# Optimization experiments

Hardware: AMD Instinct MI355X
Metric: run time of the kernel (lower is better)

Reference implementation:

```python
import jax, jax.numpy as jnp
import numpy as np

EMBED = 1024
HEADS = 16
HEAD_DIM = EMBED // HEADS
N, L = 2, 2048


def setup_inputs() -> dict:
    key = jax.random.key(0)
    ks = jax.random.split(key, 9)
    s = 0.02
    return {
        "values": jax.random.normal(ks[0], (N, L, EMBED), jnp.float32),
        "key": jax.random.normal(ks[1], (N, L, EMBED), jnp.float32),
        "query": jax.random.normal(ks[2], (N, L, EMBED), jnp.float32),
        "mask": jnp.ones((N, 1, 1, L), jnp.int32),
        "Wv": jax.random.normal(ks[3], (HEAD_DIM, HEAD_DIM), jnp.float32) * s,
        "Wk": jax.random.normal(ks[4], (HEAD_DIM, HEAD_DIM), jnp.float32) * s,
        "Wq": jax.random.normal(ks[5], (HEAD_DIM, HEAD_DIM), jnp.float32) * s,
        "bq": jax.random.normal(ks[6], (HEAD_DIM,), jnp.float32) * s,
        "Wo": jax.random.normal(ks[7], (EMBED, EMBED), jnp.float32) * s,
        "bo": jax.random.normal(ks[8], (EMBED,), jnp.float32) * s,
    }


def reference(values, key, query, mask, Wv, Wk, Wq, bq, Wo, bo):
    n, q_len, E = query.shape
    D = Wv.shape[0]
    H = E // D
    # split heads: (N, len, H, D)
    v = values.reshape(n, -1, H, D)
    k = key.reshape(n, -1, H, D)
    q = query.reshape(n, q_len, H, D)
    # per-head linear projections (torch Linear: x @ W.T [+ b])
    v = jnp.einsum("nlhd,ed->nlhe", v, Wv)
    k = jnp.einsum("nlhd,ed->nlhe", k, Wk)
    q = jnp.einsum("nlhd,ed->nlhe", q, Wq) + bq
    # scores: (N, H, q_len, k_len)
    energy = jnp.einsum("nqhd,nkhd->nhqk", q, k)
    energy = jnp.where(mask == 0, jnp.float32(-1e20), energy)
    # NOTE: original scales by sqrt(embed_size), not sqrt(head_dim)
    attn = jax.nn.softmax(energy / jnp.sqrt(jnp.float32(E)), axis=-1)
    out = jnp.einsum("nhqk,nkhd->nqhd", attn, v).reshape(n, q_len, E)
    return out @ Wo.T + bo
```

## Files before the change

### kernel.cpp

```cpp
#include <hip/hip_runtime.h>
#include <hip/hip_bf16.h>
#include <string.h>

#define NB   2
#define SEQ  2048
#define EMB  1024
#define NH   16
#define HD   64
#define QSCALE 0.045084219f

typedef __attribute__((ext_vector_type(8))) short short8;
typedef __attribute__((ext_vector_type(4))) float f32x4;

#define MFMA(a, b, c) __builtin_amdgcn_mfma_f32_16x16x32_bf16(a, b, c, 0, 0, 0)
#define EXP2(x) __builtin_amdgcn_exp2f(x)

__device__ __forceinline__ unsigned short f2bf(float x) {
    union { float f; unsigned u; } v; v.f = x;
    unsigned r = v.u + 0x7fffu + ((v.u >> 16) & 1u);
    return (unsigned short)(r >> 16);
}
__device__ __forceinline__ unsigned packbf2(float a, float b) {
    __hip_bfloat162 h = __float22bfloat162_rn(make_float2(a, b));
    unsigned u; memcpy(&u, &h, 4);
    return u;
}
__device__ __forceinline__ void gload16(const void* g, void* l) {
    __builtin_amdgcn_global_load_lds(
        (const __attribute__((address_space(1))) void*)g,
        (__attribute__((address_space(3))) void*)l, 16, 0, 0);
}

__global__ __launch_bounds__(256) void cvt_kernel(
    const float* __restrict__ Wo, const float* __restrict__ Wq,
    const float* __restrict__ Wk, const float* __restrict__ Wv,
    const int* __restrict__ mask,
    unsigned short* __restrict__ Wob, unsigned short* __restrict__ Wqb,
    unsigned short* __restrict__ Wkb, unsigned short* __restrict__ Wvb,
    unsigned short* __restrict__ Mb)
{
    const int b = blockIdx.x, tid = threadIdx.x;
    if (b < 1024) {
        int idx = b * 256 + tid;
        float4 w = ((const float4*)Wo)[idx];
        uint2 p; p.x = packbf2(w.x, w.y); p.y = packbf2(w.z, w.w);
        ((uint2*)Wob)[idx] = p;
    } else if (b < 1027) {
        const float* W = (b == 1024) ? Wq : (b == 1025) ? Wk : Wv;
        unsigned short* Wb = (b == 1024) ? Wqb : (b == 1025) ? Wkb : Wvb;
        #pragma unroll
        for (int i = 0; i < 4; ++i) {
            int idx = tid + i * 256;
            float4 w = ((const float4*)W)[idx];
            uint2 p; p.x = packbf2(w.x, w.y); p.y = packbf2(w.z, w.w);
            ((uint2*)Wb)[idx] = p;
        }
    } else {
        #pragma unroll
        for (int i = 0; i < 16; ++i) {
            int idx = tid + i * 256;
            Mb[idx] = mask[idx] ? (unsigned short)0x3F80 : (unsigned short)0;
        }
    }
}

__global__ __launch_bounds__(256) void qkv_kernel(
    const float* __restrict__ Qin, const float* __restrict__ Kin,
    const float* __restrict__ Vin,
    const unsigned short* __restrict__ Wqb, const unsigned short* __restrict__ Wkb,
    const unsigned short* __restrict__ Wvb, const float* __restrict__ bq,
    const int* __restrict__ mask,
    unsigned short* __restrict__ Qp, unsigned short* __restrict__ Kp,
    unsigned short* __restrict__ Vtp)
{
    const int lt = blockIdx.x;
    const int h  = blockIdx.y;
    const int tz = blockIdx.z;
    const int t  = tz >> 1, n = tz & 1;

    const float* X; const unsigned short* Wb;
    if (t == 0)      { X = Qin; Wb = Wqb; }
    else if (t == 1) { X = Kin; Wb = Wkb; }
    else             { X = Vin; Wb = Wvb; }

    __shared__ __align__(16) unsigned short sX[128][70];
    __shared__ __align__(16) unsigned short sT[64][136];

    const int tid = threadIdx.x, wave = tid >> 6, lane = tid & 63;
    const int ln = lane & 15, quad = lane >> 4;

    #pragma unroll
    for (int i = 0; i < 8; ++i) {
        int flat = tid + i * 256;
        int r = flat >> 4, c4 = flat & 15;
        float4 xv = *(const float4*)(X + ((size_t)(n * SEQ + lt * 128 + r)) * EMB + h * HD + c4 * 4);
        uint2 xp; xp.x = packbf2(xv.x, xv.y); xp.y = packbf2(xv.z, xv.w);
        *(uint2*)&sX[r][c4 * 4] = xp;
    }
    short8 wf0[4], wf1[4];
    #pragma unroll
    for (int nt = 0; nt < 4; ++nt) {
        wf0[nt] = *(const short8*)(Wb + (nt * 16 + ln) * HD + quad * 8);
        wf1[nt] = *(const short8*)(Wb + (nt * 16 + ln) * HD + 32 + quad * 8);
    }
    __syncthreads();

    f32x4 acc[2][4];
    #pragma unroll
    for (int set = 0; set < 2; ++set) {
        short8 af0 = *(const short8*)&sX[wave * 32 + set * 16 + ln][quad * 8];
        short8 af1 = *(const short8*)&sX[wave * 32 + set * 16 + ln][32 + quad * 8];
        #pragma unroll
        for (int nt = 0; nt < 4; ++nt) {
            f32x4 a = {0.f, 0.f, 0.f, 0.f};
            a = MFMA(af0, wf0[nt], a);
            a = MFMA(af1, wf1[nt], a);
            acc[set][nt] = a;
        }
    }

    if (t == 0) {
        #pragma unroll
        for (int nt = 0; nt < 4; ++nt) {
            float bb = bq[nt * 16 + ln];
            #pragma unroll
            for (int set = 0; set < 2; ++set)
                #pragma unroll
                for (int a = 0; a < 4; ++a)
                    acc[set][nt][a] = (acc[set][nt][a] + bb) * QSCALE;
        }
    }

    if (t < 2) {
        unsigned short* Out = (t == 0) ? Qp : Kp;
        #pragma unroll
        for (int set = 0; set < 2; ++set)
            #pragma unroll
            for (int a = 0; a < 4; ++a) {
                size_t row = (size_t)((n * NH + h) * SEQ + lt * 128 + wave * 32 + set * 16 + quad * 4 + a);
                #pragma unroll
                for (int nt = 0; nt < 4; ++nt)
                    Out[row * HD + nt * 16 + ln] = f2bf(acc[set][nt][a]);
            }
    } else {
        #pragma unroll
        for (int set = 0; set < 2; ++set)
            #pragma unroll
            for (int a = 0; a < 4; ++a) {
                int l = lt * 128 + wave * 32 + set * 16 + quad * 4 + a;
                if (mask[n * SEQ + l] == 0) {
                    #pragma unroll
                    for (int nt = 0; nt < 4; ++nt) acc[set][nt][a] = 0.f;
                }
            }
        #pragma unroll
        for (int set = 0; set < 2; ++set)
            #pragma unroll
            for (int nt = 0; nt < 4; ++nt)
                #pragma unroll
                for (int a = 0; a < 4; ++a)
                    sT[nt * 16 + ln][wave * 32 + set * 16 + quad * 4 + a] = f2bf(acc[set][nt][a]);
        __syncthreads();
        #pragma unroll
        for (int i = 0; i < 4; ++i) {
            int flat = tid + i * 256;
            int r = flat >> 4, c8 = flat & 15;
            *(float4*)(Vtp + ((size_t)((n * NH + h) * HD + r)) * SEQ + lt * 128 + c8 * 8) =
                *(const float4*)&sT[r][c8 * 8];
        }
    }
}

__global__ __launch_bounds__(256) void flash_kernel(
    const unsigned short* __restrict__ Qp, const unsigned short* __restrict__ Kp,
    const unsigned short* __restrict__ Vtp, const unsigned short* __restrict__ Mb,
    unsigned short* __restrict__ A )
{
    const int nh = blockIdx.x;
    const int qt = blockIdx.y;
    const int n  = nh >> 4, h = nh & 15;

    const int tid  = threadIdx.x;
    const int wave = tid >> 6, lane = tid & 63;
    const int ln   = lane & 15, quad = lane >> 4;
    const int ln7  = lane & 7;

    __shared__ __align__(16) unsigned short Kb[2][64 * 64];
    __shared__ __align__(16) unsigned short Vb[2][64 * 64];
    __shared__ __align__(16) unsigned short sP[4][32 * 64];
    unsigned short* sPw = sP[wave];

    const unsigned short* Qb = Qp + ((size_t)nh * SEQ + qt * 128 + wave * 32) * HD;
    short8 qf[2][2];
    #pragma unroll
    for (int set = 0; set < 2; ++set) {
        qf[set][0] = *(const short8*)(Qb + (set * 16 + ln) * HD + quad * 8);
        qf[set][1] = *(const short8*)(Qb + (set * 16 + ln) * HD + 32 + quad * 8);
    }

    const unsigned short* Kg = Kp  + (size_t)nh * SEQ * HD;
    const unsigned short* Vg = Vtp + (size_t)nh * HD * SEQ;
    const unsigned short* mk = Mb + n * SEQ;

    const int r8  = lane >> 3;
    const int swz = ((lane & 7) ^ r8) << 3;

    f32x4 o[2][4];
    #pragma unroll
    for (int s2 = 0; s2 < 2; ++s2)
        #pragma unroll
        for (int dt = 0; dt < 4; ++dt) o[s2][dt] = (f32x4){0.f, 0.f, 0.f, 0.f};
    f32x4 ol[2] = {(f32x4){0.f, 0.f, 0.f, 0.f}, (f32x4){0.f, 0.f, 0.f, 0.f}};

    #define STAGE(buf, kt_) do {                                                  \
        const unsigned short* kg_ = Kg + ((size_t)((kt_) * 64 + wave * 16 + r8)) * HD + swz; \
        const unsigned short* vg_ = Vg + ((size_t)(wave * 16 + r8)) * SEQ + (kt_) * 64 + swz; \
        unsigned short* kl_ = &Kb[buf][wave * 16 * 64];                           \
        unsigned short* vl_ = &Vb[buf][wave * 16 * 64];                           \
        gload16(kg_,            kl_);                                             \
        gload16(kg_ + 8 * HD,   kl_ + 8 * 64);                                    \
        gload16(vg_,            vl_);                                             \
        gload16(vg_ + 8 * SEQ,  vl_ + 8 * 64);                                    \
    } while (0)

    STAGE(0, 0);
    __syncthreads();
    int cur = 0;

    for (int kt = 0; kt < SEQ / 64; ++kt) {
        short8 mf0 = *(const short8*)(mk + kt * 64 + quad * 8);
        short8 mf1 = *(const short8*)(mk + kt * 64 + 32 + quad * 8);

        if (kt + 1 < SEQ / 64) STAGE(cur ^ 1, kt + 1);

        const unsigned short* Kc = Kb[cur];
        #pragma unroll
        for (int nt = 0; nt < 4; ++nt) {
            short8 kf0 = *(const short8*)&Kc[(nt * 16 + ln) * 64 + (((quad)     ^ ln7) << 3)];
            short8 kf1 = *(const short8*)&Kc[(nt * 16 + ln) * 64 + (((quad + 4) ^ ln7) << 3)];
            #pragma unroll
            for (int set = 0; set < 2; ++set) {
                f32x4 z = {0.f, 0.f, 0.f, 0.f};
                z = MFMA(kf0, qf[set][0], z);
                z = MFMA(kf1, qf[set][1], z);
                float p0 = EXP2(z[0]);
                float p1 = EXP2(z[1]);
                float p2 = EXP2(z[2]);
                float p3 = EXP2(z[3]);
                uint2 w; w.x = packbf2(p0, p1); w.y = packbf2(p2, p3);
                int prow  = set * 16 + ln;
                int chunk = nt * 2 + (quad >> 1);
                *(uint2*)&sPw[prow * 64 + ((chunk ^ ln7) << 3) + (quad & 1) * 4] = w;
            }
        }
        asm volatile("s_waitcnt lgkmcnt(0)" ::: "memory");

        const unsigned short* Vc = Vb[cur];
        short8 pf[2][2];
        #pragma unroll
        for (int set = 0; set < 2; ++set) {
            pf[set][0] = *(const short8*)&sPw[(set * 16 + ln) * 64 + (((quad)     ^ ln7) << 3)];
            pf[set][1] = *(const short8*)&sPw[(set * 16 + ln) * 64 + (((quad + 4) ^ ln7) << 3)];
        }
        #pragma unroll
        for (int set = 0; set < 2; ++set) {
            ol[set] = MFMA(pf[set][0], mf0, ol[set]);
            ol[set] = MFMA(pf[set][1], mf1, ol[set]);
        }
        #pragma unroll
        for (int dt = 0; dt < 4; ++dt) {
            short8 vf0 = *(const short8*)&Vc[(dt * 16 + ln) * 64 + (((quad)     ^ ln7) << 3)];
            short8 vf1 = *(const short8*)&Vc[(dt * 16 + ln) * 64 + (((quad + 4) ^ ln7) << 3)];
            #pragma unroll
            for (int set = 0; set < 2; ++set) {
                o[set][dt] = MFMA(pf[set][0], vf0, o[set][dt]);
                o[set][dt] = MFMA(pf[set][1], vf1, o[set][dt]);
            }
        }

        __syncthreads();
        cur ^= 1;
    }
    #undef STAGE

    #pragma unroll
    for (int set = 0; set < 2; ++set)
        #pragma unroll
        for (int a = 0; a < 4; ++a) {
            float inv = 1.0f / ol[set][a];
            size_t row = (size_t)(n * SEQ + qt * 128 + wave * 32 + set * 16 + quad * 4 + a);
            #pragma unroll
            for (int dt = 0; dt < 4; ++dt)
                A[row * EMB + h * HD + dt * 16 + ln] = f2bf(o[set][dt][a] * inv);
        }
}

__global__ __launch_bounds__(256) void outproj_kernel(
    const unsigned short* __restrict__ A, const unsigned short* __restrict__ Wob,
    const float* __restrict__ bo, float* __restrict__ Out)
{
    const int ct = blockIdx.x;
    const int rt = blockIdx.y;

    const int tid  = threadIdx.x;
    const int wave = tid >> 6, lane = tid & 63;
    const int ln   = lane & 15, quad = lane >> 4;
    const int wm   = wave >> 1, wn = wave & 1;

    __shared__ __align__(16) unsigned short sA[128][72];
    __shared__ __align__(16) unsigned short sB[128][72];

    f32x4 acc[4][4];
    #pragma unroll
    for (int i = 0; i < 4; ++i)
        #pragma unroll
        for (int j = 0; j < 4; ++j) acc[i][j] = (f32x4){0.f, 0.f, 0.f, 0.f};

    for (int kc = 0; kc < EMB / 64; ++kc) {
        __syncthreads();
        #pragma unroll
        for (int i = 0; i < 4; ++i) {
            int flat = tid + i * 256;
            int r = flat >> 3, c8 = flat & 7;
            *(float4*)&sA[r][c8 * 8] =
                *(const float4*)(A + (size_t)(rt * 128 + r) * EMB + kc * 64 + c8 * 8);
            *(float4*)&sB[r][c8 * 8] =
                *(const float4*)(Wob + (size_t)(ct * 128 + r) * EMB + kc * 64 + c8 * 8);
        }
        __syncthreads();

        #pragma unroll
        for (int ks = 0; ks < 2; ++ks) {
            short8 af[4], bf[4];
            #pragma unroll
            for (int i = 0; i < 4; ++i)
                af[i] = *(const short8*)&sA[wm * 64 + i * 16 + ln][ks * 32 + quad * 8];
            #pragma unroll
            for (int j = 0; j < 4; ++j)
                bf[j] = *(const short8*)&sB[wn * 64 + j * 16 + ln][ks * 32 + quad * 8];
            #pragma unroll
            for (int i = 0; i < 4; ++i)
                #pragma unroll
                for (int j = 0; j < 4; ++j)
                    acc[i][j] = MFMA(af[i], bf[j], acc[i][j]);
        }
    }

    #pragma unroll
    for (int j = 0; j < 4; ++j) {
        int col = ct * 128 + wn * 64 + j * 16 + ln;
        float bb = bo[col];
        #pragma unroll
        for (int i = 0; i < 4; ++i)
            #pragma unroll
            for (int a = 0; a < 4; ++a) {
                size_t row = (size_t)(rt * 128 + wm * 64 + i * 16 + quad * 4 + a);
                Out[row * EMB + col] = acc[i][j][a] + bb;
            }
    }
}

extern "C" void kernel_launch(void* const* d_in, const int* in_sizes, int n_in,
                              void* d_out, int out_size, void* d_ws, size_t ws_size,
                              hipStream_t stream) {
    const float* values = (const float*)d_in[0];
    const float* key_   = (const float*)d_in[1];
    const float* query  = (const float*)d_in[2];
    const int*   mask   = (const int*)d_in[3];
    const float* Wv     = (const float*)d_in[4];
    const float* Wk     = (const float*)d_in[5];
    const float* Wq     = (const float*)d_in[6];
    const float* bq     = (const float*)d_in[7];
    const float* Wo     = (const float*)d_in[8];
    const float* bo     = (const float*)d_in[9];
    float* out = (float*)d_out;

    const size_t NHLD = (size_t)NB * NH * SEQ * HD;

    unsigned short* ws = (unsigned short*)d_ws;
    unsigned short* Qp    = ws;
    unsigned short* Kp    = ws + NHLD;
    unsigned short* Vtp   = ws + 2 * NHLD;
    unsigned short* Aattn = ws + 3 * NHLD;
    unsigned short* Wob   = ws + 4 * NHLD;
    unsigned short* Wqb   = Wob + (size_t)EMB * EMB;
    unsigned short* Wkb   = Wqb + HD * HD;
    unsigned short* Wvb   = Wkb + HD * HD;
    unsigned short* Mb    = Wvb + HD * HD;

    cvt_kernel<<<dim3(1028), 256, 0, stream>>>(
        Wo, Wq, Wk, Wv, mask, Wob, Wqb, Wkb, Wvb, Mb);
    qkv_kernel<<<dim3(SEQ / 128, NH, 3 * NB), 256, 0, stream>>>(
        query, key_, values, Wqb, Wkb, Wvb, bq, mask, Qp, Kp, Vtp);
    flash_kernel<<<dim3(NB * NH, SEQ / 128), 256, 0, stream>>>(
        Qp, Kp, Vtp, Mb, Aattn);
    outproj_kernel<<<dim3(EMB / 128, NB * SEQ / 128), 256, 0, stream>>>(
        Aattn, Wob, bo, out);
}
```

Baseline: 192.9 us.

## Manually unroll flash loop with fixed buffers, add occupancy hint, shrink outproj tiles

The flash attention key loop is unrolled by two so that each double-buffer slot is addressed with a compile-time index, and the swizzle offsets are hoisted out of the loop. The kernel also gets a launch-bounds occupancy hint of two blocks per CU. Separately, the output projection tile is halved in rows (64x128), doubling the grid to 512 blocks for better CU fill at the cost of reloading the Wo tile more often. The occupancy hint may force register spills.

```diff
diff --git a/kernel.cpp b/kernel.cpp
--- a/kernel.cpp
+++ b/kernel.cpp
@@ -171,7 +171,7 @@
     }
 }
 
-__global__ __launch_bounds__(256) void flash_kernel(
+__global__ __launch_bounds__(256, 2) void flash_kernel(
     const unsigned short* __restrict__ Qp, const unsigned short* __restrict__ Kp,
     const unsigned short* __restrict__ Vtp, const unsigned short* __restrict__ Mb,
     unsigned short* __restrict__ A )
@@ -201,6 +201,11 @@
     const unsigned short* Kg = Kp  + (size_t)nh * SEQ * HD;
     const unsigned short* Vg = Vtp + (size_t)nh * HD * SEQ;
     const unsigned short* mk = Mb + n * SEQ;
+
+    const int kx0 = ((quad)     ^ ln7) << 3;
+    const int kx1 = ((quad + 4) ^ ln7) << 3;
+    const int pw0 = ((quad >> 1) ^ ln7) << 3;
+    const int pwb = (quad & 1) * 4;
 
     const int r8  = lane >> 3;
     const int swz = ((lane & 7) ^ r8) << 3;
@@ -223,65 +228,65 @@
         gload16(vg_ + 8 * SEQ,  vl_ + 8 * 64);                                    \
     } while (0)
 
+    #define COMPUTE(BUF, KT) do {                                                 \
+        short8 mf0 = *(const short8*)(mk + (KT) * 64 + quad * 8);                 \
+        short8 mf1 = *(const short8*)(mk + (KT) * 64 + 32 + quad * 8);            \
+        _Pragma("unroll")                                                         \
+        for (int nt = 0; nt < 4; ++nt) {                                          \
+            short8 kf0 = *(const short8*)&Kb[BUF][(nt * 16 + ln) * 64 + kx0];     \
+            short8 kf1 = *(const short8*)&Kb[BUF][(nt * 16 + ln) * 64 + kx1];     \
+            _Pragma("unroll")                                                     \
+            for (int set = 0; set < 2; ++set) {                                   \
+                f32x4 z = {0.f, 0.f, 0.f, 0.f};                                   \
+                z = MFMA(kf0, qf[set][0], z);                                     \
+                z = MFMA(kf1, qf[set][1], z);                                     \
+                float p0 = EXP2(z[0]);                                            \
+                float p1 = EXP2(z[1]);                                            \
+                float p2 = EXP2(z[2]);                                            \
+                float p3 = EXP2(z[3]);                                            \
+                uint2 w; w.x = packbf2(p0, p1); w.y = packbf2(p2, p3);            \
+                *(uint2*)&sPw[(set * 16 + ln) * 64 + (pw0 ^ (nt * 2 << 3)) + pwb] = w; \
+            }                                                                     \
+        }                                                                         \
+        asm volatile("s_waitcnt lgkmcnt(0)" ::: "memory");                        \
+        short8 pf[2][2];                                                          \
+        _Pragma("unroll")                                                         \
+        for (int set = 0; set < 2; ++set) {                                       \
+            pf[set][0] = *(const short8*)&sPw[(set * 16 + ln) * 64 + kx0];        \
+            pf[set][1] = *(const short8*)&sPw[(set * 16 + ln) * 64 + kx1];        \
+        }                                                                         \
+        _Pragma("unroll")                                                         \
+        for (int set = 0; set < 2; ++set) {                                       \
+            ol[set] = MFMA(pf[set][0], mf0, ol[set]);                             \
+            ol[set] = MFMA(pf[set][1], mf1, ol[set]);                             \
+        }                                                                         \
+        _Pragma("unroll")                                                         \
+        for (int dt = 0; dt < 4; ++dt) {                                          \
+            short8 vf0 = *(const short8*)&Vb[BUF][(dt * 16 + ln) * 64 + kx0];     \
+            short8 vf1 = *(const short8*)&Vb[BUF][(dt * 16 + ln) * 64 + kx1];     \
+            _Pragma("unroll")                                                     \
+            for (int set = 0; set < 2; ++set) {                                   \
+                o[set][dt] = MFMA(pf[set][0], vf0, o[set][dt]);                   \
+                o[set][dt] = MFMA(pf[set][1], vf1, o[set][dt]);                   \
+            }                                                                     \
+        }                                                                         \
+    } while (0)
+
     STAGE(0, 0);
     __syncthreads();
-    int cur = 0;
-
-    for (int kt = 0; kt < SEQ / 64; ++kt) {
-        short8 mf0 = *(const short8*)(mk + kt * 64 + quad * 8);
-        short8 mf1 = *(const short8*)(mk + kt * 64 + 32 + quad * 8);
-
-        if (kt + 1 < SEQ / 64) STAGE(cur ^ 1, kt + 1);
-
-        const unsigned short* Kc = Kb[cur];
-        #pragma unroll
-        for (int nt = 0; nt < 4; ++nt) {
-            short8 kf0 = *(const short8*)&Kc[(nt * 16 + ln) * 64 + (((quad)     ^ ln7) << 3)];
-            short8 kf1 = *(const short8*)&Kc[(nt * 16 + ln) * 64 + (((quad + 4) ^ ln7) << 3)];
-            #pragma unroll
-            for (int set = 0; set < 2; ++set) {
-                f32x4 z = {0.f, 0.f, 0.f, 0.f};
-                z = MFMA(kf0, qf[set][0], z);
-                z = MFMA(kf1, qf[set][1], z);
-                float p0 = EXP2(z[0]);
-                float p1 = EXP2(z[1]);
-                float p2 = EXP2(z[2]);
-                float p3 = EXP2(z[3]);
-                uint2 w; w.x = packbf2(p0, p1); w.y = packbf2(p2, p3);
-                int prow  = set * 16 + ln;
-                int chunk = nt * 2 + (quad >> 1);
-                *(uint2*)&sPw[prow * 64 + ((chunk ^ ln7) << 3) + (quad & 1) * 4] = w;
-            }
-        }
-        asm volatile("s_waitcnt lgkmcnt(0)" ::: "memory");
-
-        const unsigned short* Vc = Vb[cur];
-        short8 pf[2][2];
-        #pragma unroll
-        for (int set = 0; set < 2; ++set) {
-            pf[set][0] = *(const short8*)&sPw[(set * 16 + ln) * 64 + (((quad)     ^ ln7) << 3)];
-            pf[set][1] = *(const short8*)&sPw[(set * 16 + ln) * 64 + (((quad + 4) ^ ln7) << 3)];
-        }
-        #pragma unroll
-        for (int set = 0; set < 2; ++set) {
-            ol[set] = MFMA(pf[set][0], mf0, ol[set]);
-            ol[set] = MFMA(pf[set][1], mf1, ol[set]);
-        }
-        #pragma unroll
-        for (int dt = 0; dt < 4; ++dt) {
-            short8 vf0 = *(const short8*)&Vc[(dt * 16 + ln) * 64 + (((quad)     ^ ln7) << 3)];
-            short8 vf1 = *(const short8*)&Vc[(dt * 16 + ln) * 64 + (((quad + 4) ^ ln7) << 3)];
-            #pragma unroll
-            for (int set = 0; set < 2; ++set) {
-                o[set][dt] = MFMA(pf[set][0], vf0, o[set][dt]);
-                o[set][dt] = MFMA(pf[set][1], vf1, o[set][dt]);
-            }
-        }
-
+
+    #pragma unroll 1
+    for (int kt = 0; kt < SEQ / 64; kt += 2) {
+        STAGE(1, kt + 1);
+        COMPUTE(0, kt);
         __syncthreads();
-        cur ^= 1;
+        if (kt + 2 < SEQ / 64) STAGE(0, kt + 2);
+        COMPUTE(1, kt + 1);
+        __syncthreads();
     }
     #undef STAGE
+    #undef COMPUTE
+
 
     #pragma unroll
     for (int set = 0; set < 2; ++set)
@@ -307,23 +312,28 @@
     const int ln   = lane & 15, quad = lane >> 4;
     const int wm   = wave >> 1, wn = wave & 1;
 
-    __shared__ __align__(16) unsigned short sA[128][72];
+    __shared__ __align__(16) unsigned short sA[64][72];
     __shared__ __align__(16) unsigned short sB[128][72];
 
-    f32x4 acc[4][4];
-    #pragma unroll
-    for (int i = 0; i < 4; ++i)
+    f32x4 acc[2][4];
+    #pragma unroll
+    for (int i = 0; i < 2; ++i)
         #pragma unroll
         for (int j = 0; j < 4; ++j) acc[i][j] = (f32x4){0.f, 0.f, 0.f, 0.f};
 
     for (int kc = 0; kc < EMB / 64; ++kc) {
         __syncthreads();
+        #pragma unroll
+        for (int i = 0; i < 2; ++i) {
+            int flat = tid + i * 256;
+            int r = flat >> 3, c8 = flat & 7;
+            *(float4*)&sA[r][c8 * 8] =
+                *(const float4*)(A + (size_t)(rt * 64 + r) * EMB + kc * 64 + c8 * 8);
+        }
         #pragma unroll
         for (int i = 0; i < 4; ++i) {
             int flat = tid + i * 256;
             int r = flat >> 3, c8 = flat & 7;
-            *(float4*)&sA[r][c8 * 8] =
-                *(const float4*)(A + (size_t)(rt * 128 + r) * EMB + kc * 64 + c8 * 8);
             *(float4*)&sB[r][c8 * 8] =
                 *(const float4*)(Wob + (size_t)(ct * 128 + r) * EMB + kc * 64 + c8 * 8);
         }
@@ -331,15 +341,15 @@
 
         #pragma unroll
         for (int ks = 0; ks < 2; ++ks) {
-            short8 af[4], bf[4];
-            #pragma unroll
-            for (int i = 0; i < 4; ++i)
-                af[i] = *(const short8*)&sA[wm * 64 + i * 16 + ln][ks * 32 + quad * 8];
+            short8 af[2], bf[4];
+            #pragma unroll
+            for (int i = 0; i < 2; ++i)
+                af[i] = *(const short8*)&sA[wm * 32 + i * 16 + ln][ks * 32 + quad * 8];
             #pragma unroll
             for (int j = 0; j < 4; ++j)
                 bf[j] = *(const short8*)&sB[wn * 64 + j * 16 + ln][ks * 32 + quad * 8];
             #pragma unroll
-            for (int i = 0; i < 4; ++i)
+            for (int i = 0; i < 2; ++i)
                 #pragma unroll
                 for (int j = 0; j < 4; ++j)
                     acc[i][j] = MFMA(af[i], bf[j], acc[i][j]);
@@ -351,10 +361,10 @@
         int col = ct * 128 + wn * 64 + j * 16 + ln;
         float bb = bo[col];
         #pragma unroll
-        for (int i = 0; i < 4; ++i)
+        for (int i = 0; i < 2; ++i)
             #pragma unroll
             for (int a = 0; a < 4; ++a) {
-                size_t row = (size_t)(rt * 128 + wm * 64 + i * 16 + quad * 4 + a);
+                size_t row = (size_t)(rt * 64 + wm * 32 + i * 16 + quad * 4 + a);
                 Out[row * EMB + col] = acc[i][j][a] + bb;
             }
     }
@@ -394,6 +404,6 @@
         query, key_, values, Wqb, Wkb, Wvb, bq, mask, Qp, Kp, Vtp);
     flash_kernel<<<dim3(NB * NH, SEQ / 128), 256, 0, stream>>>(
         Qp, Kp, Vtp, Mb, Aattn);
-    outproj_kernel<<<dim3(EMB / 128, NB * SEQ / 128), 256, 0, stream>>>(
+    outproj_kernel<<<dim3(EMB / 128, NB * SEQ / 64), 256, 0, stream>>>(
         Aattn, Wob, bo, out);
 }
```

Measured after the change: 203.3 us. 1.05x slower.
